# Kernel optimization log

Measured on AMD Instinct MI355X. Metric: run time of the kernel, lower is better.

## Reference

```python
import jax, jax.numpy as jnp
import numpy as np

N, E, M = 4096, 65536, 16   # nodes, edges, channel multiplicity per degree
MID = 32                    # RadialFunc hidden width (SE3-Transformer default)
EPS = 1e-5                  # BatchNorm1d eps
DEGS = [0, 1]
PAIRS = [(0, 0), (0, 1), (1, 0), (1, 1)]  # (d_in, d_out)


def _bn_relu(x, g, b):
    # BatchNorm1d in training mode (biased batch stats over edges) + ReLU
    mu = x.mean(0, keepdims=True)
    var = ((x - mu) ** 2).mean(0, keepdims=True)
    return jax.nn.relu((x - mu) / jnp.sqrt(var + EPS) * g + b)


def _radial(feat, w1, b1, g1, be1, w2, b2, g2, be2, w3, b3, nf):
    # RadialFunc: Linear-BN-ReLU, Linear-BN-ReLU, Linear -> [E, nc_out, 1, nc_in, 1, nf]
    y = _bn_relu(feat @ w1 + b1, g1, be1)
    y = _bn_relu(y @ w2 + b2, g2, be2)
    y = y @ w3 + b3
    return y.reshape(-1, M, 1, M, 1, nf)


def _forward(h0, h1, r, basis00, basis01, basis10, basis11,
             rw1, rb1, rg1, rbe1, rw2, rb2, rg2, rbe2,
             w3_00, b3_00, w3_01, b3_01, w3_10, b3_10, w3_11, b3_11,
             Wself0, Wself1, edge_src, edge_dst):
    h = {0: h0, 1: h1}
    basis = {(0, 0): basis00, (0, 1): basis01, (1, 0): basis10, (1, 1): basis11}
    w3b3 = {(0, 0): (w3_00, b3_00), (0, 1): (w3_01, b3_01),
            (1, 0): (w3_10, b3_10), (1, 1): (w3_11, b3_11)}
    Wself = {0: Wself0, 1: Wself1}
    # PairwiseConv: per-edge kernel = sum_f R * basis  -> [E, M, 2do+1, M, 2di+1]
    kern = {}
    for p, (di, do) in enumerate(PAIRS):
        nf = 2 * min(di, do) + 1
        w3, b3 = w3b3[(di, do)]
        R = _radial(r, rw1[p], rb1[p], rg1[p], rbe1[p],
                    rw2[p], rb2[p], rg2[p], rbe2[p], w3, b3, nf)
        kern[(di, do)] = (R * basis[(di, do)]).sum(-1)
    cnt = jnp.maximum(
        jax.ops.segment_sum(jnp.ones((E,), h0.dtype), edge_dst, num_segments=N), 1.0)
    outs = []
    for do in DEGS:
        msg = jnp.zeros((E, M, 2 * do + 1), h0.dtype)
        for di in DEGS:
            # per-edge small matmul: kernel @ gathered source feature
            msg = msg + jnp.einsum('eopiq,eiq->eop', kern[(di, do)], h[di][edge_src])
        # self-interaction, flavor='skip': add W @ destination feature per edge
        msg = msg + jnp.einsum('mi,eip->emp', Wself[do][0], h[do][edge_dst])
        s = jax.ops.segment_sum(msg, edge_dst, num_segments=N)  # scatter-mean
        outs.append(s / cnt[:, None, None])
    return tuple(outs)


def setup_inputs() -> dict:
    key = jax.random.key(0)
    ks = jax.random.split(key, 20)
    nrm = lambda k, sh, s=1.0: jax.random.normal(k, sh, jnp.float32) * s
    return {
        'h0': nrm(ks[0], (N, M, 1)),
        'h1': nrm(ks[1], (N, M, 3)),
        'r': jax.random.uniform(ks[2], (E, 1), jnp.float32),
        'basis00': nrm(ks[3], (E, 1, 1, 1, 1, 1)),
        'basis01': nrm(ks[4], (E, 1, 3, 1, 1, 1)),
        'basis10': nrm(ks[5], (E, 1, 1, 1, 3, 1)),
        'basis11': nrm(ks[6], (E, 1, 3, 1, 3, 3)),
        'rw1': nrm(ks[7], (4, 1, MID)),
        'rb1': jnp.zeros((4, MID), jnp.float32),
        'rg1': jnp.ones((4, MID), jnp.float32),
        'rbe1': jnp.zeros((4, MID), jnp.float32),
        'rw2': nrm(ks[8], (4, MID, MID), 1.0 / np.sqrt(MID)),
        'rb2': jnp.zeros((4, MID), jnp.float32),
        'rg2': jnp.ones((4, MID), jnp.float32),
        'rbe2': jnp.zeros((4, MID), jnp.float32),
        'w3_00': nrm(ks[9], (MID, M * M), 1.0 / np.sqrt(MID)),
        'b3_00': jnp.zeros((M * M,), jnp.float32),
        'w3_01': nrm(ks[10], (MID, M * M), 1.0 / np.sqrt(MID)),
        'b3_01': jnp.zeros((M * M,), jnp.float32),
        'w3_10': nrm(ks[11], (MID, M * M), 1.0 / np.sqrt(MID)),
        'b3_10': jnp.zeros((M * M,), jnp.float32),
        'w3_11': nrm(ks[12], (MID, M * M * 3), 1.0 / np.sqrt(MID)),
        'b3_11': jnp.zeros((M * M * 3,), jnp.float32),
        'Wself0': nrm(ks[13], (1, M, M), 1.0 / np.sqrt(M)),
        'Wself1': nrm(ks[14], (1, M, M), 1.0 / np.sqrt(M)),
        'edge_src': jax.random.randint(ks[15], (E,), 0, N),
        'edge_dst': jax.random.randint(ks[16], (E,), 0, N),
    }


def reference(h0, h1, r, basis00, basis01, basis10, basis11,
              rw1, rb1, rg1, rbe1, rw2, rb2, rg2, rbe2,
              w3_00, b3_00, w3_01, b3_01, w3_10, b3_10, w3_11, b3_11,
              Wself0, Wself1, edge_src, edge_dst):
    return _forward(h0, h1, r, basis00, basis01, basis10, basis11,
                    rw1, rb1, rg1, rbe1, rw2, rb2, rg2, rbe2,
                    w3_00, b3_00, w3_01, b3_01, w3_10, b3_10, w3_11, b3_11,
                    Wself0, Wself1, edge_src, edge_dst)
```

## Files before the change

kernel.cpp:

```cpp
#include <hip/hip_runtime.h>

#define N_NODES 4096
#define N_EDGES 65536
#define MID 32
#define BN_EPS 1e-5f

#define WS_RSUM    0
#define WS_RSUMSQ  1
#define WS_ALPHA1  272
#define WS_BETA1   400
#define WS_A2      528
#define WS_S2      656
#define WS_BP      784
#define WS_GRAM    5120
#define WS_SUMY    9216
#define WS_W2T     17664
#define WS_PWL     24576
#define WS_MSG_F   262144
#define WS_U00     4456448
#define WS_U01     4521984
#define WS_V10     4587520
#define WS_W11     4784128
#define WS_DEG_I   1024
#define WS_CUR_I   9344
#define WS_OFFS_I  13440
#define WS_ELIST_I 65536
#define WSB_WA     524288
#define WSB_WB     557056
#define WSB_WC     573440

typedef short bf16x8 __attribute__((ext_vector_type(8)));
typedef float f32x4  __attribute__((ext_vector_type(4)));

__device__ __forceinline__ unsigned short f2bf(float x) {
    unsigned u = __float_as_uint(x);
    u += 0x7fffu + ((u >> 16) & 1u);
    return (unsigned short)(u >> 16);
}

__device__ __forceinline__ int wimg_idx(int col, int k) {
    return col * 32 + ((((col >> 1) + (k >> 3)) & 3) << 3) + (k & 7);
}

__global__ void __launch_bounds__(256) k_pre(const float* __restrict__ rw2,
        const float* __restrict__ w300, const float* __restrict__ w301,
        const float* __restrict__ w310, const float* __restrict__ w311,
        const float* __restrict__ bw300, const float* __restrict__ bw301,
        const float* __restrict__ bw310, const float* __restrict__ bw311,
        const float* __restrict__ r, const int* __restrict__ edst,
        const float* __restrict__ h0, const float* __restrict__ h1,
        float* __restrict__ wsf) {
    if (blockIdx.x < 128) {
        int t = blockIdx.x * 256 + threadIdx.x;
        char* wsb = (char*)wsf;
        if (t < 4096) {
            int p = t >> 10, rem = t & 1023, c = rem >> 5, k = rem & 31;
            wsf[WS_W2T + t] = rw2[(p << 10) + (k << 5) + c];
        }
        if (t < 16384) {
            int col = t >> 5, k = t & 31;
            float v = (col < 256) ? w300[(k << 8) + col] : w310[(k << 8) + (col - 256)];
            ((unsigned short*)(wsb + WSB_WA))[wimg_idx(col, k)] = f2bf(v);
        }
        if (t < 8192) {
            int col = t >> 5, k = t & 31;
            ((unsigned short*)(wsb + WSB_WB))[wimg_idx(col, k)] = f2bf(w301[(k << 8) + col]);
        }
        if (t < 24576) {
            int col = t >> 5, k = t & 31;
            int f = col >> 8, rem = col & 255;
            ((unsigned short*)(wsb + WSB_WC))[wimg_idx(col, k)] = f2bf(w311[k * 768 + rem * 3 + f]);
        }
    } else if (blockIdx.x < 384) {
        int e = (blockIdx.x - 128) * 256 + threadIdx.x;
        float v = r[e];
        atomicAdd(((int*)wsf) + WS_DEG_I + edst[e], 1);
        float s = v, ss = v * v;
#pragma unroll
        for (int mk = 32; mk >= 1; mk >>= 1) {
            s  += __shfl_xor(s,  mk, 64);
            ss += __shfl_xor(ss, mk, 64);
        }
        __shared__ float ls[4], lss[4];
        int lane = threadIdx.x & 63, wv = threadIdx.x >> 6;
        if (lane == 0) { ls[wv] = s; lss[wv] = ss; }
        __syncthreads();
        if (threadIdx.x == 0) {
            atomicAdd(wsf + WS_RSUM,   ls[0] + ls[1] + ls[2] + ls[3]);
            atomicAdd(wsf + WS_RSUMSQ, lss[0] + lss[1] + lss[2] + lss[3]);
        }
    } else {
        int g = (blockIdx.x - 384) * 256 + threadIdx.x;
        int n = g >> 4, mo = g & 15;
        float h1r[48];
#pragma unroll
        for (int j = 0; j < 48; ++j) h1r[j] = h1[n * 48 + j];
        float s00 = 0.f, s01 = 0.f;
#pragma unroll
        for (int mi = 0; mi < 16; ++mi) {
            float hv = h0[n * 16 + mi];
            s00 += bw300[mo * 16 + mi] * hv;
            s01 += bw301[mo * 16 + mi] * hv;
        }
        wsf[WS_U00 + n * 16 + mo] = s00;
        wsf[WS_U01 + n * 16 + mo] = s01;
#pragma unroll
        for (int q = 0; q < 3; ++q) {
            float sv = 0.f;
#pragma unroll
            for (int mi = 0; mi < 16; ++mi)
                sv += bw310[mo * 16 + mi] * h1r[mi * 3 + q];
            wsf[WS_V10 + n * 48 + q * 16 + mo] = sv;
        }
#pragma unroll
        for (int f = 0; f < 3; ++f)
#pragma unroll
            for (int q = 0; q < 3; ++q) {
                float sv = 0.f;
#pragma unroll
                for (int mi = 0; mi < 16; ++mi)
                    sv += bw311[(mo * 16 + mi) * 3 + f] * h1r[mi * 3 + q];
                wsf[WS_W11 + n * 144 + (f * 3 + q) * 16 + mo] = sv;
            }
    }
}

__global__ void __launch_bounds__(512) k_gram(const float* __restrict__ r,
        const float* __restrict__ rw1, const float* __restrict__ rg1,
        const float* __restrict__ rbe1, float* __restrict__ wsf) {
    int t = threadIdx.x;
    int wv = t >> 6, lane = t & 63;
    int quad = lane >> 4, lq = lane & 15;
    int p  = __builtin_amdgcn_readfirstlane(wv & 3);
    int mt = __builtin_amdgcn_readfirstlane(wv >> 2);
    float mu_r  = wsf[WS_RSUM] * (1.f / N_EDGES);
    float var_r = wsf[WS_RSUMSQ] * (1.f / N_EDGES) - mu_r * mu_r;
    float al[2], be[2];
#pragma unroll
    for (int hh = 0; hh < 2; ++hh) {
        int ch = p * 32 + hh * 16 + lq;
        float w1 = rw1[ch];
        float a = w1 * rg1[ch] * rsqrtf(w1 * w1 * var_r + BN_EPS);
        al[hh] = a;
        be[hh] = rbe1[ch] - a * mu_r;
    }
    bf16x8 ones;
#pragma unroll
    for (int j = 0; j < 8; ++j) ones[j] = (short)0x3F80;
    f32x4 accG0 = {0.f, 0.f, 0.f, 0.f};
    f32x4 accG1 = {0.f, 0.f, 0.f, 0.f};
    f32x4 accS  = {0.f, 0.f, 0.f, 0.f};
    int ebase = blockIdx.x * 512;
#pragma unroll 1
    for (int ks = 0; ks < 16; ++ks) {
        const float* rp = r + ebase + ks * 32 + quad * 8;
        float4 ra = *(const float4*)(rp);
        float4 rb = *(const float4*)(rp + 4);
        float rv[8] = {ra.x, ra.y, ra.z, ra.w, rb.x, rb.y, rb.z, rb.w};
        bf16x8 fr0, fr1;
#pragma unroll
        for (int j = 0; j < 8; ++j) {
            fr0[j] = (short)f2bf(fmaxf(0.f, al[0] * rv[j] + be[0]));
            fr1[j] = (short)f2bf(fmaxf(0.f, al[1] * rv[j] + be[1]));
        }
        bf16x8 fA = mt ? fr1 : fr0;
        accG0 = __builtin_amdgcn_mfma_f32_16x16x32_bf16(fA, fr0, accG0, 0, 0, 0);
        accG1 = __builtin_amdgcn_mfma_f32_16x16x32_bf16(fA, fr1, accG1, 0, 0, 0);
        accS  = __builtin_amdgcn_mfma_f32_16x16x32_bf16(fA, ones, accS,  0, 0, 0);
    }
    float* G = wsf + WS_GRAM + p * 1024;
#pragma unroll
    for (int reg = 0; reg < 4; ++reg) {
        int k1 = mt * 16 + quad * 4 + reg;
        atomicAdd(&G[k1 * 32 + lq],      accG0[reg]);
        atomicAdd(&G[k1 * 32 + 16 + lq], accG1[reg]);
    }
    if (lq == 0) {
#pragma unroll
        for (int reg = 0; reg < 4; ++reg)
            atomicAdd(wsf + WS_SUMY + p * 32 + mt * 16 + quad * 4 + reg, accS[reg]);
    }
}

__global__ void __launch_bounds__(1024) k_fs(const float* __restrict__ rw1,
        const float* __restrict__ rg1, const float* __restrict__ rbe1,
        const float* __restrict__ rg2, const float* __restrict__ rbe2,
        const float* __restrict__ rb2, float* __restrict__ wsf) {
    int t = threadIdx.x;
    __shared__ float sG[4096];
    __shared__ float sW[128 * 33];
    __shared__ float sSumy[128];
    __shared__ float sal[128], sbe[128], sbp[128];
    __shared__ float ssal[128], ssbe[128];
    __shared__ int   ssk[128];
    __shared__ int   sdata[1024];
#pragma unroll
    for (int i = 0; i < 4; ++i) sG[t + i * 1024] = wsf[WS_GRAM + t + i * 1024];
#pragma unroll
    for (int i = 0; i < 4; ++i) {
        int idx = t + i * 1024;
        sW[(idx >> 5) * 33 + (idx & 31)] = wsf[WS_W2T + idx];
    }
    if (t < 128) sSumy[t] = wsf[WS_SUMY + t];
    __syncthreads();

    float a2 = 0.f, s2v = 0.f;
    if (t < 128) {
        float mu_r  = wsf[WS_RSUM] * (1.f / N_EDGES);
        float var_r = wsf[WS_RSUMSQ] * (1.f / N_EDGES) - mu_r * mu_r;
        float w1 = rw1[t];
        float al = w1 * rg1[t] * rsqrtf(w1 * w1 * var_r + BN_EPS);
        float be = rbe1[t] - al * mu_r;
        sal[t] = al;
        sbe[t] = be;
        float bp = (al != 0.f) ? (-be / al) : 3.0e38f;
        sbp[t] = bp;
        wsf[WS_BP + t] = bp;
        int p = t >> 5;
        const float* w = sW + t * 33;
        const float* G = sG + p * 1024;
        float invE = 1.f / N_EDGES;
        float s1 = 0.f;
#pragma unroll
        for (int k = 0; k < 32; ++k) s1 += w[k] * (sSumy[p * 32 + k] * invE);
        float q = 0.f;
#pragma unroll 1
        for (int k1 = 0; k1 < 32; ++k1) {
            float a = 0.f;
#pragma unroll
            for (int k2 = 0; k2 < 32; ++k2) a += w[k2] * G[k1 * 32 + k2];
            q += w[k1] * a;
        }
        float var = q * invE - s1 * s1;
        a2 = rg2[t] * rsqrtf(var + BN_EPS);
        float mu2 = rb2[t] + s1;
        s2v = rbe2[t] - mu2 * a2;
    }
    __syncthreads();
    if (t < 128) {
        int p = t >> 5, k = t & 31;
        float mybp = sbp[t];
        int rank = 0;
#pragma unroll
        for (int k2 = 0; k2 < 32; ++k2) {
            float b2 = sbp[p * 32 + k2];
            rank += ((b2 < mybp) || (b2 == mybp && k2 < k)) ? 1 : 0;
        }
        ssal[p * 32 + rank] = sal[t];
        ssbe[p * 32 + rank] = sbe[t];
        ssk [p * 32 + rank] = k;
    }
    __syncthreads();
    if (t < 128) {
        int p = t >> 5, c = t & 31;
        const float* w = sW + t * 33;
        float A = 0.f, B = rb2[t];
#pragma unroll
        for (int k = 0; k < 32; ++k) {
            float ak = sal[p * 32 + k], bk = sbe[p * 32 + k], wk = w[k];
            bool neg = ak < 0.f;
            bool zc  = (ak == 0.f) && (bk > 0.f);
            A += neg ? ak * wk : 0.f;
            B += (neg || zc) ? bk * wk : 0.f;
        }
        float* outp = wsf + WS_PWL + p * 2112 + c;
        outp[0]  = a2 * A;
        outp[32] = a2 * B + s2v;
#pragma unroll
        for (int j = 1; j <= 32; ++j) {
            float ak = ssal[p * 32 + j - 1], bk = ssbe[p * 32 + j - 1];
            int sk = ssk[p * 32 + j - 1];
            float wk = w[sk];
            float sg = (ak > 0.f) ? 1.f : ((ak < 0.f) ? -1.f : 0.f);
            A += sg * ak * wk;
            B += sg * bk * wk;
            outp[j * 64]      = a2 * A;
            outp[j * 64 + 32] = a2 * B + s2v;
        }
    }

    const int* deg = ((const int*)wsf) + WS_DEG_I;
    int* offs = ((int*)wsf) + WS_OFFS_I;
    int* cur  = ((int*)wsf) + WS_CUR_I;
    int v0 = deg[t * 4], v1 = deg[t * 4 + 1], v2 = deg[t * 4 + 2], v3 = deg[t * 4 + 3];
    sdata[t] = v0 + v1 + v2 + v3;
    __syncthreads();
    for (int off = 1; off < 1024; off <<= 1) {
        int x = sdata[t];
        int y = (t >= off) ? sdata[t - off] : 0;
        __syncthreads();
        sdata[t] = x + y;
        __syncthreads();
    }
    int excl = (t == 0) ? 0 : sdata[t - 1];
    int o0 = excl, o1 = excl + v0, o2 = o1 + v1, o3 = o2 + v2;
    offs[t * 4] = o0;     cur[t * 4] = o0;
    offs[t * 4 + 1] = o1; cur[t * 4 + 1] = o1;
    offs[t * 4 + 2] = o2; cur[t * 4 + 2] = o2;
    offs[t * 4 + 3] = o3; cur[t * 4 + 3] = o3;
    if (t == 1023) offs[4096] = sdata[1023];
}

__global__ void __launch_bounds__(256) k_bucket(const int* __restrict__ edst,
                                                float* __restrict__ wsf) {
    int e = blockIdx.x * 256 + threadIdx.x;
    int d = edst[e];
    int* cur   = ((int*)wsf) + WS_CUR_I;
    int* elist = ((int*)wsf) + WS_ELIST_I;
    int pos = atomicAdd(&cur[d], 1);
    elist[pos] = e;
}

__device__ __forceinline__ void y2_pwl16(int p, int el, int c0, float rv,
                                         const float* __restrict__ wsf, char* dst) {
    int j = 0;
#pragma unroll
    for (int k4 = 0; k4 < 8; ++k4) {
        float4 bp = *(const float4*)(wsf + WS_BP + p * 32 + k4 * 4);
        j += (rv > bp.x) + (rv > bp.y) + (rv > bp.z) + (rv > bp.w);
    }
    const float* ta = wsf + WS_PWL + p * 2112 + j * 64 + c0;
    unsigned short h[16];
#pragma unroll
    for (int cc = 0; cc < 16; ++cc)
        h[cc] = f2bf(fmaxf(0.f, ta[cc] * rv + ta[32 + cc]));
#pragma unroll
    for (int q = 0; q < 2; ++q) {
        int4 pk;
        pk.x = (int)h[q * 8 + 0] | ((int)h[q * 8 + 1] << 16);
        pk.y = (int)h[q * 8 + 2] | ((int)h[q * 8 + 3] << 16);
        pk.z = (int)h[q * 8 + 4] | ((int)h[q * 8 + 5] << 16);
        pk.w = (int)h[q * 8 + 6] | ((int)h[q * 8 + 7] << 16);
        int jc = (c0 >> 3) + q;
        int slot = ((el >> 1) + jc) & 3;
        *(int4*)(dst + el * 64 + slot * 16) = pk;
    }
}

__global__ void __launch_bounds__(512, 2) k_msg(const float* __restrict__ r,
        const float* __restrict__ h0, const float* __restrict__ h1,
        const float* __restrict__ b00, const float* __restrict__ b01,
        const float* __restrict__ b10, const float* __restrict__ b11,
        const int* __restrict__ esrc,
        const float* __restrict__ wsf, float* __restrict__ msg) {
    extern __shared__ char smem[];
    short* w3s = (short*)smem;
    const char* wsb = (const char*)wsf;
    int t = threadIdx.x;
    int wv = t >> 6, lane = t & 63;
    int quad = lane >> 4, lq = lane & 15;
    int eb = blockIdx.x << 8;
    int woff = (((lq >> 1) + quad) & 3) << 3;
    int yoff = (((lq >> 1) + quad) & 3) << 4;
    float d1c[2][4];

    {
        const float4* src = (const float4*)(wsb + WSB_WA);
        float4* dst = (float4*)smem;
#pragma unroll
        for (int i = 0; i < 4; ++i) dst[i * 512 + t] = src[i * 512 + t];
    }
    {
        int p = __builtin_amdgcn_readfirstlane((t >> 8) * 2);
        int el = t & 255;
        float rv = r[eb + el];
        char* dst = smem + 32768 + (t >> 8) * 16384;
        y2_pwl16(p, el, 0, rv, wsf, dst);
        y2_pwl16(p, el, 16, rv, wsf, dst);
    }
    __syncthreads();
#pragma unroll
    for (int g2 = 0; g2 < 2; ++g2) {
        int el = (wv * 2 + g2) * 16 + lq;
        int e = eb + el;
        int s = esrc[e];
        bf16x8 bf0 = *(const bf16x8*)(smem + 32768 + el * 64 + yoff);
        bf16x8 bf2 = *(const bf16x8*)(smem + 49152 + el * 64 + yoff);
        float4 h0q = *(const float4*)(h0 + s * 16 + quad * 4);
        float4 hv0 = *(const float4*)(h1 + s * 48 + quad * 12);
        float4 hv1 = *(const float4*)(h1 + s * 48 + quad * 12 + 4);
        float4 hv2 = *(const float4*)(h1 + s * 48 + quad * 12 + 8);
        float b00v = b00[e];
        float bq0 = b10[e * 3 + 0], bq1 = b10[e * 3 + 1], bq2 = b10[e * 3 + 2];
        float gq0 = bq0 * hv0.x + bq1 * hv0.y + bq2 * hv0.z;
        float gq1 = bq0 * hv0.w + bq1 * hv1.x + bq2 * hv1.y;
        float gq2 = bq0 * hv1.z + bq1 * hv1.w + bq2 * hv2.x;
        float gq3 = bq0 * hv2.y + bq1 * hv2.z + bq2 * hv2.w;
        float4 u00q = *(const float4*)(wsf + WS_U00 + s * 16 + quad * 4);
        float a0[4];
#pragma unroll
        for (int rr = 0; rr < 4; ++rr) a0[rr] = b00v * ((const float*)&u00q)[rr];
#pragma unroll
        for (int q = 0; q < 3; ++q) {
            float4 vq = *(const float4*)(wsf + WS_V10 + s * 48 + q * 16 + quad * 4);
            float bq = (q == 0) ? bq0 : (q == 1) ? bq1 : bq2;
#pragma unroll
            for (int rr = 0; rr < 4; ++rr) a0[rr] += bq * ((const float*)&vq)[rr];
        }
#pragma unroll
        for (int m = 0; m < 16; ++m) {
            bf16x8 af = *(const bf16x8*)(w3s + (m * 16 + lq) * 32 + woff);
            f32x4 dd = __builtin_amdgcn_mfma_f32_16x16x32_bf16(af, bf0, (f32x4){0.f,0.f,0.f,0.f}, 0, 0, 0);
            float partial = dd[0] * h0q.x + dd[1] * h0q.y + dd[2] * h0q.z + dd[3] * h0q.w;
            partial += __shfl_xor(partial, 16);
            partial += __shfl_xor(partial, 32);
            a0[m & 3] += (quad == (m >> 2)) ? b00v * partial : 0.f;
        }
#pragma unroll
        for (int m = 0; m < 16; ++m) {
            bf16x8 af = *(const bf16x8*)(w3s + (256 + m * 16 + lq) * 32 + woff);
            f32x4 dd = __builtin_amdgcn_mfma_f32_16x16x32_bf16(af, bf2, (f32x4){0.f,0.f,0.f,0.f}, 0, 0, 0);
            float partial = dd[0] * gq0 + dd[1] * gq1 + dd[2] * gq2 + dd[3] * gq3;
            partial += __shfl_xor(partial, 16);
            partial += __shfl_xor(partial, 32);
            a0[m & 3] += (quad == (m >> 2)) ? partial : 0.f;
        }
        float4 w = {a0[0], a0[1], a0[2], a0[3]};
        *(float4*)(msg + (size_t)e * 64 + quad * 4) = w;
    }
    __syncthreads();

    {
        const float4* src = (const float4*)(wsb + WSB_WB);
        float4* dst = (float4*)smem;
#pragma unroll
        for (int i = 0; i < 2; ++i) dst[i * 512 + t] = src[i * 512 + t];
    }
    {
        int el = t & 255, c0 = (t >> 8) * 16;
        y2_pwl16(1, el, c0, r[eb + el], wsf, smem + 16384);
    }
    __syncthreads();
#pragma unroll
    for (int g2 = 0; g2 < 2; ++g2) {
        int el = (wv * 2 + g2) * 16 + lq;
        int e = eb + el;
        int s = esrc[e];
        bf16x8 bf1 = *(const bf16x8*)(smem + 16384 + el * 64 + yoff);
        float4 h0q = *(const float4*)(h0 + s * 16 + quad * 4);
        float d1[4] = {0.f, 0.f, 0.f, 0.f};
#pragma unroll
        for (int m = 0; m < 16; ++m) {
            bf16x8 af = *(const bf16x8*)(w3s + (m * 16 + lq) * 32 + woff);
            f32x4 dd = __builtin_amdgcn_mfma_f32_16x16x32_bf16(af, bf1, (f32x4){0.f,0.f,0.f,0.f}, 0, 0, 0);
            float partial = dd[0] * h0q.x + dd[1] * h0q.y + dd[2] * h0q.z + dd[3] * h0q.w;
            partial += __shfl_xor(partial, 16);
            partial += __shfl_xor(partial, 32);
            d1[m & 3] += (quad == (m >> 2)) ? partial : 0.f;
        }
#pragma unroll
        for (int rr = 0; rr < 4; ++rr) d1c[g2][rr] = d1[rr];
    }
    __syncthreads();

    {
        const float4* src = (const float4*)(wsb + WSB_WC);
        float4* dst = (float4*)smem;
#pragma unroll
        for (int i = 0; i < 6; ++i) dst[i * 512 + t] = src[i * 512 + t];
    }
    {
        int el = t & 255, c0 = (t >> 8) * 16;
        y2_pwl16(3, el, c0, r[eb + el], wsf, smem + 49152);
    }
    __syncthreads();
#pragma unroll
    for (int g2 = 0; g2 < 2; ++g2) {
        int el = (wv * 2 + g2) * 16 + lq;
        int e = eb + el;
        int s = esrc[e];
        bf16x8 bf3 = *(const bf16x8*)(smem + 49152 + el * 64 + yoff);
        float4 hv0 = *(const float4*)(h1 + s * 48 + quad * 12);
        float4 hv1 = *(const float4*)(h1 + s * 48 + quad * 12 + 4);
        float4 hv2 = *(const float4*)(h1 + s * 48 + quad * 12 + 8);
        float h1v[4][3] = {{hv0.x, hv0.y, hv0.z}, {hv0.w, hv1.x, hv1.y},
                           {hv1.z, hv1.w, hv2.x}, {hv2.y, hv2.z, hv2.w}};
        float bo0 = b01[e * 3 + 0], bo1 = b01[e * 3 + 1], bo2 = b01[e * 3 + 2];
        float4 u01q = *(const float4*)(wsf + WS_U01 + s * 16 + quad * 4);
        float m1[4][3];
#pragma unroll
        for (int rr = 0; rr < 4; ++rr) {
            float u = d1c[g2][rr] + ((const float*)&u01q)[rr];
            m1[rr][0] = bo0 * u; m1[rr][1] = bo1 * u; m1[rr][2] = bo2 * u;
        }
#pragma unroll
        for (int f = 0; f < 3; ++f)
#pragma unroll
            for (int q = 0; q < 3; ++q) {
                float4 wq = *(const float4*)(wsf + WS_W11 + s * 144 + (f * 3 + q) * 16 + quad * 4);
#pragma unroll
                for (int o = 0; o < 3; ++o) {
                    float bas = b11[e * 27 + o * 9 + q * 3 + f];
#pragma unroll
                    for (int rr = 0; rr < 4; ++rr) m1[rr][o] += bas * ((const float*)&wq)[rr];
                }
            }
#pragma unroll
        for (int f = 0; f < 3; ++f) {
            float Tf[4][3];
#pragma unroll
            for (int o = 0; o < 3; ++o) {
                float bv0 = b11[e * 27 + o * 9 + 0 + f];
                float bv1 = b11[e * 27 + o * 9 + 3 + f];
                float bv2 = b11[e * 27 + o * 9 + 6 + f];
#pragma unroll
                for (int rr = 0; rr < 4; ++rr)
                    Tf[rr][o] = h1v[rr][0] * bv0 + h1v[rr][1] * bv1 + h1v[rr][2] * bv2;
            }
#pragma unroll
            for (int m = 0; m < 16; ++m) {
                int colb = f * 256 + m * 16 + lq;
                bf16x8 af = *(const bf16x8*)(w3s + colb * 32 + woff);
                f32x4 dd = __builtin_amdgcn_mfma_f32_16x16x32_bf16(af, bf3, (f32x4){0.f,0.f,0.f,0.f}, 0, 0, 0);
#pragma unroll
                for (int o = 0; o < 3; ++o) {
                    float po = dd[0] * Tf[0][o] + dd[1] * Tf[1][o] + dd[2] * Tf[2][o] + dd[3] * Tf[3][o];
                    po += __shfl_xor(po, 16);
                    po += __shfl_xor(po, 32);
                    m1[m & 3][o] += (quad == (m >> 2)) ? po : 0.f;
                }
            }
        }
        float* base = msg + (size_t)e * 64 + 16 + quad * 12;
        float4 w0 = {m1[0][0], m1[0][1], m1[0][2], m1[1][0]};
        float4 w1 = {m1[1][1], m1[1][2], m1[2][0], m1[2][1]};
        float4 w2 = {m1[2][2], m1[3][0], m1[3][1], m1[3][2]};
        *(float4*)(base)     = w0;
        *(float4*)(base + 4) = w1;
        *(float4*)(base + 8) = w2;
    }
}

__global__ void __launch_bounds__(256) k_gather(const float* __restrict__ h0,
        const float* __restrict__ h1, const float* __restrict__ Wself0,
        const float* __restrict__ Wself1, const float* __restrict__ wsf,
        float* __restrict__ out) {
    int wv = threadIdx.x >> 6, lane = threadIdx.x & 63;
    int n = blockIdx.x * 4 + wv;
    const int* offs  = ((const int*)wsf) + WS_OFFS_I;
    const int* elist = ((const int*)wsf) + WS_ELIST_I;
    const float* msg = wsf + WS_MSG_F;
    int start = offs[n], end = offs[n + 1];
    int deg = end - start;
    float acc = 0.f;
    for (int j0 = 0; j0 < deg; j0 += 64) {
        int cnt = min(64, deg - j0);
        int eidv = (j0 + lane < deg) ? elist[start + j0 + lane] : 0;
        int jj = 0;
        for (; jj + 3 < cnt; jj += 4) {
            int e0 = __shfl(eidv, jj), e1 = __shfl(eidv, jj + 1);
            int e2 = __shfl(eidv, jj + 2), e3 = __shfl(eidv, jj + 3);
            float v0 = msg[(size_t)e0 * 64 + lane];
            float v1 = msg[(size_t)e1 * 64 + lane];
            float v2 = msg[(size_t)e2 * 64 + lane];
            float v3 = msg[(size_t)e3 * 64 + lane];
            acc += (v0 + v1) + (v2 + v3);
        }
        for (; jj < cnt; ++jj) {
            int eid = __shfl(eidv, jj);
            acc += msg[(size_t)eid * 64 + lane];
        }
    }
    float self = 0.f;
    if (lane < 16) {
        int m = lane;
#pragma unroll
        for (int i = 0; i < 16; ++i) self += Wself0[m * 16 + i] * h0[n * 16 + i];
    } else {
        int idx = lane - 16; int m = idx / 3, o = idx % 3;
#pragma unroll
        for (int i = 0; i < 16; ++i) self += Wself1[m * 16 + i] * h1[n * 48 + i * 3 + o];
    }
    float c = (float)(deg > 0 ? deg : 1);
    float res = acc / c + (deg > 0 ? self : 0.f);
    if (lane < 16) out[n * 16 + lane] = res;
    else           out[65536 + n * 48 + (lane - 16)] = res;
}

extern "C" void kernel_launch(void* const* d_in, const int* in_sizes, int n_in,
                              void* d_out, int out_size, void* d_ws, size_t ws_size,
                              hipStream_t stream) {
    const float* h0   = (const float*)d_in[0];
    const float* h1   = (const float*)d_in[1];
    const float* r    = (const float*)d_in[2];
    const float* b00  = (const float*)d_in[3];
    const float* b01  = (const float*)d_in[4];
    const float* b10  = (const float*)d_in[5];
    const float* b11  = (const float*)d_in[6];
    const float* rw1  = (const float*)d_in[7];
    const float* rg1  = (const float*)d_in[9];
    const float* rbe1 = (const float*)d_in[10];
    const float* rw2  = (const float*)d_in[11];
    const float* rb2  = (const float*)d_in[12];
    const float* rg2  = (const float*)d_in[13];
    const float* rbe2 = (const float*)d_in[14];
    const float* w300 = (const float*)d_in[15];
    const float* bw300= (const float*)d_in[16];
    const float* w301 = (const float*)d_in[17];
    const float* bw301= (const float*)d_in[18];
    const float* w310 = (const float*)d_in[19];
    const float* bw310= (const float*)d_in[20];
    const float* w311 = (const float*)d_in[21];
    const float* bw311= (const float*)d_in[22];
    const float* Wself0 = (const float*)d_in[23];
    const float* Wself1 = (const float*)d_in[24];
    const int* esrc = (const int*)d_in[25];
    const int* edst = (const int*)d_in[26];
    float* out = (float*)d_out;
    float* wsf = (float*)d_ws;
    float* msg = wsf + WS_MSG_F;

    static bool attr_set = false;
    if (!attr_set) {
        hipFuncSetAttribute((const void*)k_msg,
                            hipFuncAttributeMaxDynamicSharedMemorySize, 65536);
        attr_set = true;
    }

    hipMemsetAsync(d_ws, 0, 37376, stream);

    k_pre<<<640, 256, 0, stream>>>(rw2, w300, w301, w310, w311,
                                   bw300, bw301, bw310, bw311, r, edst, h0, h1, wsf);
    k_gram<<<128, 512, 0, stream>>>(r, rw1, rg1, rbe1, wsf);
    k_fs<<<1, 1024, 0, stream>>>(rw1, rg1, rbe1, rg2, rbe2, rb2, wsf);
    k_bucket<<<256, 256, 0, stream>>>(edst, wsf);
    k_msg<<<256, 512, 65536, stream>>>(r, h0, h1, b00, b01, b10, b11,
                                       esrc, wsf, msg);
    k_gather<<<1024, 256, 0, stream>>>(h0, h1, Wself0, Wself1, wsf, out);
}
```

Measured before the change: 233.6 us.

## Split message kernel into three per-pair kernels to cut register pressure

The monolithic per-edge message kernel is split into three kernels, one per group of degree pairs. The d1 partials now go straight to the degree-1 message slots, and the (1,1) kernel reads them back and accumulates into them. Loops are kept rolled (unroll 1) and the basis values are loaded once per f, with the aim of lowering register usage and improving occupancy. In exchange it adds two extra launches, repeated index and feature gathers, and an extra read-modify-write of the degree-1 message region through global memory. The grid is only 256 blocks, so higher occupancy may not help much.

```diff
diff --git a/kernel.cpp b/kernel.cpp
--- a/kernel.cpp
+++ b/kernel.cpp
@@ -337,10 +337,10 @@
     }
 }
 
-__global__ void __launch_bounds__(512, 2) k_msg(const float* __restrict__ r,
+
+__global__ void __launch_bounds__(512, 2) k_msgA(const float* __restrict__ r,
         const float* __restrict__ h0, const float* __restrict__ h1,
-        const float* __restrict__ b00, const float* __restrict__ b01,
-        const float* __restrict__ b10, const float* __restrict__ b11,
+        const float* __restrict__ b00, const float* __restrict__ b10,
         const int* __restrict__ esrc,
         const float* __restrict__ wsf, float* __restrict__ msg) {
     extern __shared__ char smem[];
@@ -352,8 +352,6 @@
     int eb = blockIdx.x << 8;
     int woff = (((lq >> 1) + quad) & 3) << 3;
     int yoff = (((lq >> 1) + quad) & 3) << 4;
-    float d1c[2][4];
-
     {
         const float4* src = (const float4*)(wsb + WSB_WA);
         float4* dst = (float4*)smem;
@@ -369,7 +367,7 @@
         y2_pwl16(p, el, 16, rv, wsf, dst);
     }
     __syncthreads();
-#pragma unroll
+#pragma unroll 1
     for (int g2 = 0; g2 < 2; ++g2) {
         int el = (wv * 2 + g2) * 16 + lq;
         int e = eb + el;
@@ -418,8 +416,21 @@
         float4 w = {a0[0], a0[1], a0[2], a0[3]};
         *(float4*)(msg + (size_t)e * 64 + quad * 4) = w;
     }
-    __syncthreads();
-
+}
+
+__global__ void __launch_bounds__(512, 2) k_msgB(const float* __restrict__ r,
+        const float* __restrict__ h0, const float* __restrict__ b01,
+        const int* __restrict__ esrc,
+        const float* __restrict__ wsf, float* __restrict__ msg) {
+    extern __shared__ char smem[];
+    short* w3s = (short*)smem;
+    const char* wsb = (const char*)wsf;
+    int t = threadIdx.x;
+    int wv = t >> 6, lane = t & 63;
+    int quad = lane >> 4, lq = lane & 15;
+    int eb = blockIdx.x << 8;
+    int woff = (((lq >> 1) + quad) & 3) << 3;
+    int yoff = (((lq >> 1) + quad) & 3) << 4;
     {
         const float4* src = (const float4*)(wsb + WSB_WB);
         float4* dst = (float4*)smem;
@@ -448,11 +459,33 @@
             partial += __shfl_xor(partial, 32);
             d1[m & 3] += (quad == (m >> 2)) ? partial : 0.f;
         }
-#pragma unroll
-        for (int rr = 0; rr < 4; ++rr) d1c[g2][rr] = d1[rr];
-    }
-    __syncthreads();
-
+        float bo0 = b01[e * 3 + 0], bo1 = b01[e * 3 + 1], bo2 = b01[e * 3 + 2];
+        float4 u01q = *(const float4*)(wsf + WS_U01 + s * 16 + quad * 4);
+        float u0 = d1[0] + u01q.x, u1 = d1[1] + u01q.y;
+        float u2 = d1[2] + u01q.z, u3 = d1[3] + u01q.w;
+        float* base = msg + (size_t)e * 64 + 16 + quad * 12;
+        float4 w0 = {bo0 * u0, bo1 * u0, bo2 * u0, bo0 * u1};
+        float4 w1 = {bo1 * u1, bo2 * u1, bo0 * u2, bo1 * u2};
+        float4 w2 = {bo2 * u2, bo0 * u3, bo1 * u3, bo2 * u3};
+        *(float4*)(base)     = w0;
+        *(float4*)(base + 4) = w1;
+        *(float4*)(base + 8) = w2;
+    }
+}
+
+__global__ void __launch_bounds__(512, 2) k_msgC(const float* __restrict__ r,
+        const float* __restrict__ h1, const float* __restrict__ b11,
+        const int* __restrict__ esrc,
+        const float* __restrict__ wsf, float* __restrict__ msg) {
+    extern __shared__ char smem[];
+    short* w3s = (short*)smem;
+    const char* wsb = (const char*)wsf;
+    int t = threadIdx.x;
+    int wv = t >> 6, lane = t & 63;
+    int quad = lane >> 4, lq = lane & 15;
+    int eb = blockIdx.x << 8;
+    int woff = (((lq >> 1) + quad) & 3) << 3;
+    int yoff = (((lq >> 1) + quad) & 3) << 4;
     {
         const float4* src = (const float4*)(wsb + WSB_WC);
         float4* dst = (float4*)smem;
@@ -464,7 +497,7 @@
         y2_pwl16(3, el, c0, r[eb + el], wsf, smem + 49152);
     }
     __syncthreads();
-#pragma unroll
+#pragma unroll 1
     for (int g2 = 0; g2 < 2; ++g2) {
         int el = (wv * 2 + g2) * 16 + lq;
         int e = eb + el;
@@ -475,38 +508,34 @@
         float4 hv2 = *(const float4*)(h1 + s * 48 + quad * 12 + 8);
         float h1v[4][3] = {{hv0.x, hv0.y, hv0.z}, {hv0.w, hv1.x, hv1.y},
                            {hv1.z, hv1.w, hv2.x}, {hv2.y, hv2.z, hv2.w}};
-        float bo0 = b01[e * 3 + 0], bo1 = b01[e * 3 + 1], bo2 = b01[e * 3 + 2];
-        float4 u01q = *(const float4*)(wsf + WS_U01 + s * 16 + quad * 4);
         float m1[4][3];
 #pragma unroll
-        for (int rr = 0; rr < 4; ++rr) {
-            float u = d1c[g2][rr] + ((const float*)&u01q)[rr];
-            m1[rr][0] = bo0 * u; m1[rr][1] = bo1 * u; m1[rr][2] = bo2 * u;
-        }
-#pragma unroll
-        for (int f = 0; f < 3; ++f)
+        for (int rr = 0; rr < 4; ++rr)
+#pragma unroll
+            for (int o = 0; o < 3; ++o) m1[rr][o] = 0.f;
+#pragma unroll 1
+        for (int f = 0; f < 3; ++f) {
+            float bv[3][3];
+#pragma unroll
+            for (int o = 0; o < 3; ++o)
+#pragma unroll
+                for (int q = 0; q < 3; ++q)
+                    bv[o][q] = b11[(size_t)e * 27 + o * 9 + q * 3 + f];
 #pragma unroll
             for (int q = 0; q < 3; ++q) {
                 float4 wq = *(const float4*)(wsf + WS_W11 + s * 144 + (f * 3 + q) * 16 + quad * 4);
 #pragma unroll
-                for (int o = 0; o < 3; ++o) {
-                    float bas = b11[e * 27 + o * 9 + q * 3 + f];
-#pragma unroll
-                    for (int rr = 0; rr < 4; ++rr) m1[rr][o] += bas * ((const float*)&wq)[rr];
-                }
+                for (int o = 0; o < 3; ++o)
+#pragma unroll
+                    for (int rr = 0; rr < 4; ++rr)
+                        m1[rr][o] += bv[o][q] * ((const float*)&wq)[rr];
             }
-#pragma unroll
-        for (int f = 0; f < 3; ++f) {
             float Tf[4][3];
 #pragma unroll
-            for (int o = 0; o < 3; ++o) {
-                float bv0 = b11[e * 27 + o * 9 + 0 + f];
-                float bv1 = b11[e * 27 + o * 9 + 3 + f];
-                float bv2 = b11[e * 27 + o * 9 + 6 + f];
+            for (int o = 0; o < 3; ++o)
 #pragma unroll
                 for (int rr = 0; rr < 4; ++rr)
-                    Tf[rr][o] = h1v[rr][0] * bv0 + h1v[rr][1] * bv1 + h1v[rr][2] * bv2;
-            }
+                    Tf[rr][o] = h1v[rr][0] * bv[o][0] + h1v[rr][1] * bv[o][1] + h1v[rr][2] * bv[o][2];
 #pragma unroll
             for (int m = 0; m < 16; ++m) {
                 int colb = f * 256 + m * 16 + lq;
@@ -522,9 +551,12 @@
             }
         }
         float* base = msg + (size_t)e * 64 + 16 + quad * 12;
-        float4 w0 = {m1[0][0], m1[0][1], m1[0][2], m1[1][0]};
-        float4 w1 = {m1[1][1], m1[1][2], m1[2][0], m1[2][1]};
-        float4 w2 = {m1[2][2], m1[3][0], m1[3][1], m1[3][2]};
+        float4 r0 = *(const float4*)(base);
+        float4 r1 = *(const float4*)(base + 4);
+        float4 r2 = *(const float4*)(base + 8);
+        float4 w0 = {m1[0][0] + r0.x, m1[0][1] + r0.y, m1[0][2] + r0.z, m1[1][0] + r0.w};
+        float4 w1 = {m1[1][1] + r1.x, m1[1][2] + r1.y, m1[2][0] + r1.z, m1[2][1] + r1.w};
+        float4 w2 = {m1[2][2] + r2.x, m1[3][0] + r2.y, m1[3][1] + r2.z, m1[3][2] + r2.w};
         *(float4*)(base)     = w0;
         *(float4*)(base + 4) = w1;
         *(float4*)(base + 8) = w2;
@@ -612,7 +644,11 @@
 
     static bool attr_set = false;
     if (!attr_set) {
-        hipFuncSetAttribute((const void*)k_msg,
+        hipFuncSetAttribute((const void*)k_msgA,
+                            hipFuncAttributeMaxDynamicSharedMemorySize, 65536);
+        hipFuncSetAttribute((const void*)k_msgB,
+                            hipFuncAttributeMaxDynamicSharedMemorySize, 32768);
+        hipFuncSetAttribute((const void*)k_msgC,
                             hipFuncAttributeMaxDynamicSharedMemorySize, 65536);
         attr_set = true;
     }
@@ -624,7 +660,8 @@
     k_gram<<<128, 512, 0, stream>>>(r, rw1, rg1, rbe1, wsf);
     k_fs<<<1, 1024, 0, stream>>>(rw1, rg1, rbe1, rg2, rbe2, rb2, wsf);
     k_bucket<<<256, 256, 0, stream>>>(edst, wsf);
-    k_msg<<<256, 512, 65536, stream>>>(r, h0, h1, b00, b01, b10, b11,
-                                       esrc, wsf, msg);
+    k_msgA<<<256, 512, 65536, stream>>>(r, h0, h1, b00, b10, esrc, wsf, msg);
+    k_msgB<<<256, 512, 32768, stream>>>(r, h0, b01, esrc, wsf, msg);
+    k_msgC<<<256, 512, 65536, stream>>>(r, h1, b11, esrc, wsf, msg);
     k_gather<<<1024, 256, 0, stream>>>(h0, h1, Wself0, Wself1, wsf, out);
 }
```

Result: faster. 217.1 us (-7.1%).

## Split message kernel into two phases and fold edge bucketing into first

Applied to the files above, without the earlier changes.

The edge-bucketing kernel is folded into the first message kernel, which cuts one launch. The single three-phase message kernel is split into k_msgA (degree-0 output) and k_msgBC (degree-1 output). k_msgBC loads the B and C weight tiles and both radial activations at once into 96KB of shared memory, which drops two intra-kernel barrier and reload stages, and loops are set to unroll 1 to reduce register pressure. In exchange, k_msgBC recomputes some gathers, the extra launch adds overhead, and the larger shared-memory footprint may lower occupancy.

```diff
diff --git a/kernel.cpp b/kernel.cpp
--- a/kernel.cpp
+++ b/kernel.cpp
@@ -301,16 +301,6 @@
     if (t == 1023) offs[4096] = sdata[1023];
 }
 
-__global__ void __launch_bounds__(256) k_bucket(const int* __restrict__ edst,
-                                                float* __restrict__ wsf) {
-    int e = blockIdx.x * 256 + threadIdx.x;
-    int d = edst[e];
-    int* cur   = ((int*)wsf) + WS_CUR_I;
-    int* elist = ((int*)wsf) + WS_ELIST_I;
-    int pos = atomicAdd(&cur[d], 1);
-    elist[pos] = e;
-}
-
 __device__ __forceinline__ void y2_pwl16(int p, int el, int c0, float rv,
                                          const float* __restrict__ wsf, char* dst) {
     int j = 0;
@@ -337,12 +327,11 @@
     }
 }
 
-__global__ void __launch_bounds__(512, 2) k_msg(const float* __restrict__ r,
+__global__ void __launch_bounds__(512, 2) k_msgA(const float* __restrict__ r,
         const float* __restrict__ h0, const float* __restrict__ h1,
-        const float* __restrict__ b00, const float* __restrict__ b01,
-        const float* __restrict__ b10, const float* __restrict__ b11,
-        const int* __restrict__ esrc,
-        const float* __restrict__ wsf, float* __restrict__ msg) {
+        const float* __restrict__ b00, const float* __restrict__ b10,
+        const int* __restrict__ esrc, const int* __restrict__ edst,
+        float* __restrict__ wsf, float* __restrict__ msg) {
     extern __shared__ char smem[];
     short* w3s = (short*)smem;
     const char* wsb = (const char*)wsf;
@@ -352,8 +341,13 @@
     int eb = blockIdx.x << 8;
     int woff = (((lq >> 1) + quad) & 3) << 3;
     int yoff = (((lq >> 1) + quad) & 3) << 4;
-    float d1c[2][4];
-
+    if (t < 256) {
+        int e2 = eb + t;
+        int* cur   = ((int*)wsf) + WS_CUR_I;
+        int* elist = ((int*)wsf) + WS_ELIST_I;
+        int pos = atomicAdd(&cur[edst[e2]], 1);
+        elist[pos] = e2;
+    }
     {
         const float4* src = (const float4*)(wsb + WSB_WA);
         float4* dst = (float4*)smem;
@@ -369,7 +363,7 @@
         y2_pwl16(p, el, 16, rv, wsf, dst);
     }
     __syncthreads();
-#pragma unroll
+#pragma unroll 1
     for (int g2 = 0; g2 < 2; ++g2) {
         int el = (wv * 2 + g2) * 16 + lq;
         int e = eb + el;
@@ -418,99 +412,98 @@
         float4 w = {a0[0], a0[1], a0[2], a0[3]};
         *(float4*)(msg + (size_t)e * 64 + quad * 4) = w;
     }
-    __syncthreads();
-
+}
+
+__global__ void __launch_bounds__(512, 2) k_msgBC(const float* __restrict__ r,
+        const float* __restrict__ h0, const float* __restrict__ h1,
+        const float* __restrict__ b01, const float* __restrict__ b11,
+        const int* __restrict__ esrc,
+        const float* __restrict__ wsf, float* __restrict__ msg) {
+    extern __shared__ char smem[];
+    short* w3sB = (short*)smem;
+    short* w3sC = (short*)(smem + 16384);
+    const char* wsb = (const char*)wsf;
+    int t = threadIdx.x;
+    int wv = t >> 6, lane = t & 63;
+    int quad = lane >> 4, lq = lane & 15;
+    int eb = blockIdx.x << 8;
+    int woff = (((lq >> 1) + quad) & 3) << 3;
+    int yoff = (((lq >> 1) + quad) & 3) << 4;
     {
-        const float4* src = (const float4*)(wsb + WSB_WB);
-        float4* dst = (float4*)smem;
-#pragma unroll
-        for (int i = 0; i < 2; ++i) dst[i * 512 + t] = src[i * 512 + t];
+        const float4* srcB = (const float4*)(wsb + WSB_WB);
+        float4* dstB = (float4*)smem;
+#pragma unroll
+        for (int i = 0; i < 2; ++i) dstB[i * 512 + t] = srcB[i * 512 + t];
+        const float4* srcC = (const float4*)(wsb + WSB_WC);
+        float4* dstC = (float4*)(smem + 16384);
+#pragma unroll
+        for (int i = 0; i < 6; ++i) dstC[i * 512 + t] = srcC[i * 512 + t];
     }
     {
         int el = t & 255, c0 = (t >> 8) * 16;
-        y2_pwl16(1, el, c0, r[eb + el], wsf, smem + 16384);
+        float rv = r[eb + el];
+        y2_pwl16(1, el, c0, rv, wsf, smem + 65536);
+        y2_pwl16(3, el, c0, rv, wsf, smem + 81920);
     }
     __syncthreads();
-#pragma unroll
+#pragma unroll 1
     for (int g2 = 0; g2 < 2; ++g2) {
         int el = (wv * 2 + g2) * 16 + lq;
         int e = eb + el;
         int s = esrc[e];
-        bf16x8 bf1 = *(const bf16x8*)(smem + 16384 + el * 64 + yoff);
+        bf16x8 bf1 = *(const bf16x8*)(smem + 65536 + el * 64 + yoff);
         float4 h0q = *(const float4*)(h0 + s * 16 + quad * 4);
         float d1[4] = {0.f, 0.f, 0.f, 0.f};
 #pragma unroll
         for (int m = 0; m < 16; ++m) {
-            bf16x8 af = *(const bf16x8*)(w3s + (m * 16 + lq) * 32 + woff);
+            bf16x8 af = *(const bf16x8*)(w3sB + (m * 16 + lq) * 32 + woff);
             f32x4 dd = __builtin_amdgcn_mfma_f32_16x16x32_bf16(af, bf1, (f32x4){0.f,0.f,0.f,0.f}, 0, 0, 0);
             float partial = dd[0] * h0q.x + dd[1] * h0q.y + dd[2] * h0q.z + dd[3] * h0q.w;
             partial += __shfl_xor(partial, 16);
             partial += __shfl_xor(partial, 32);
             d1[m & 3] += (quad == (m >> 2)) ? partial : 0.f;
         }
-#pragma unroll
-        for (int rr = 0; rr < 4; ++rr) d1c[g2][rr] = d1[rr];
-    }
-    __syncthreads();
-
-    {
-        const float4* src = (const float4*)(wsb + WSB_WC);
-        float4* dst = (float4*)smem;
-#pragma unroll
-        for (int i = 0; i < 6; ++i) dst[i * 512 + t] = src[i * 512 + t];
-    }
-    {
-        int el = t & 255, c0 = (t >> 8) * 16;
-        y2_pwl16(3, el, c0, r[eb + el], wsf, smem + 49152);
-    }
-    __syncthreads();
-#pragma unroll
-    for (int g2 = 0; g2 < 2; ++g2) {
-        int el = (wv * 2 + g2) * 16 + lq;
-        int e = eb + el;
-        int s = esrc[e];
-        bf16x8 bf3 = *(const bf16x8*)(smem + 49152 + el * 64 + yoff);
+        float bo0 = b01[e * 3 + 0], bo1 = b01[e * 3 + 1], bo2 = b01[e * 3 + 2];
+        float4 u01q = *(const float4*)(wsf + WS_U01 + s * 16 + quad * 4);
+        float m1[4][3];
+#pragma unroll
+        for (int rr = 0; rr < 4; ++rr) {
+            float u = d1[rr] + ((const float*)&u01q)[rr];
+            m1[rr][0] = bo0 * u; m1[rr][1] = bo1 * u; m1[rr][2] = bo2 * u;
+        }
+        bf16x8 bf3 = *(const bf16x8*)(smem + 81920 + el * 64 + yoff);
         float4 hv0 = *(const float4*)(h1 + s * 48 + quad * 12);
         float4 hv1 = *(const float4*)(h1 + s * 48 + quad * 12 + 4);
         float4 hv2 = *(const float4*)(h1 + s * 48 + quad * 12 + 8);
         float h1v[4][3] = {{hv0.x, hv0.y, hv0.z}, {hv0.w, hv1.x, hv1.y},
                            {hv1.z, hv1.w, hv2.x}, {hv2.y, hv2.z, hv2.w}};
-        float bo0 = b01[e * 3 + 0], bo1 = b01[e * 3 + 1], bo2 = b01[e * 3 + 2];
-        float4 u01q = *(const float4*)(wsf + WS_U01 + s * 16 + quad * 4);
-        float m1[4][3];
-#pragma unroll
-        for (int rr = 0; rr < 4; ++rr) {
-            float u = d1c[g2][rr] + ((const float*)&u01q)[rr];
-            m1[rr][0] = bo0 * u; m1[rr][1] = bo1 * u; m1[rr][2] = bo2 * u;
-        }
-#pragma unroll
-        for (int f = 0; f < 3; ++f)
+#pragma unroll 1
+        for (int f = 0; f < 3; ++f) {
+            float bv[3][3];
+#pragma unroll
+            for (int o = 0; o < 3; ++o)
+#pragma unroll
+                for (int q = 0; q < 3; ++q)
+                    bv[o][q] = b11[(size_t)e * 27 + o * 9 + q * 3 + f];
 #pragma unroll
             for (int q = 0; q < 3; ++q) {
                 float4 wq = *(const float4*)(wsf + WS_W11 + s * 144 + (f * 3 + q) * 16 + quad * 4);
 #pragma unroll
-                for (int o = 0; o < 3; ++o) {
-                    float bas = b11[e * 27 + o * 9 + q * 3 + f];
-#pragma unroll
-                    for (int rr = 0; rr < 4; ++rr) m1[rr][o] += bas * ((const float*)&wq)[rr];
-                }
+                for (int o = 0; o < 3; ++o)
+#pragma unroll
+                    for (int rr = 0; rr < 4; ++rr)
+                        m1[rr][o] += bv[o][q] * ((const float*)&wq)[rr];
             }
-#pragma unroll
-        for (int f = 0; f < 3; ++f) {
             float Tf[4][3];
 #pragma unroll
-            for (int o = 0; o < 3; ++o) {
-                float bv0 = b11[e * 27 + o * 9 + 0 + f];
-                float bv1 = b11[e * 27 + o * 9 + 3 + f];
-                float bv2 = b11[e * 27 + o * 9 + 6 + f];
+            for (int o = 0; o < 3; ++o)
 #pragma unroll
                 for (int rr = 0; rr < 4; ++rr)
-                    Tf[rr][o] = h1v[rr][0] * bv0 + h1v[rr][1] * bv1 + h1v[rr][2] * bv2;
-            }
+                    Tf[rr][o] = h1v[rr][0] * bv[o][0] + h1v[rr][1] * bv[o][1] + h1v[rr][2] * bv[o][2];
 #pragma unroll
             for (int m = 0; m < 16; ++m) {
                 int colb = f * 256 + m * 16 + lq;
-                bf16x8 af = *(const bf16x8*)(w3s + colb * 32 + woff);
+                bf16x8 af = *(const bf16x8*)(w3sC + colb * 32 + woff);
                 f32x4 dd = __builtin_amdgcn_mfma_f32_16x16x32_bf16(af, bf3, (f32x4){0.f,0.f,0.f,0.f}, 0, 0, 0);
 #pragma unroll
                 for (int o = 0; o < 3; ++o) {
@@ -612,8 +605,10 @@
 
     static bool attr_set = false;
     if (!attr_set) {
-        hipFuncSetAttribute((const void*)k_msg,
+        hipFuncSetAttribute((const void*)k_msgA,
                             hipFuncAttributeMaxDynamicSharedMemorySize, 65536);
+        hipFuncSetAttribute((const void*)k_msgBC,
+                            hipFuncAttributeMaxDynamicSharedMemorySize, 98304);
         attr_set = true;
     }
 
@@ -623,8 +618,7 @@
                                    bw300, bw301, bw310, bw311, r, edst, h0, h1, wsf);
     k_gram<<<128, 512, 0, stream>>>(r, rw1, rg1, rbe1, wsf);
     k_fs<<<1, 1024, 0, stream>>>(rw1, rg1, rbe1, rg2, rbe2, rb2, wsf);
-    k_bucket<<<256, 256, 0, stream>>>(edst, wsf);
-    k_msg<<<256, 512, 65536, stream>>>(r, h0, h1, b00, b01, b10, b11,
-                                       esrc, wsf, msg);
+    k_msgA<<<256, 512, 65536, stream>>>(r, h0, h1, b00, b10, esrc, edst, wsf, msg);
+    k_msgBC<<<256, 512, 98304, stream>>>(r, h0, h1, b01, b11, esrc, wsf, msg);
     k_gather<<<1024, 256, 0, stream>>>(h0, h1, Wself0, Wself1, wsf, out);
 }
```

New measurement: 216.2 us, median of 3. 1.08x faster.
